# Performance work log

Measured on AMD Instinct MI355X. Metric: run time of the kernel, lower is better.

The kernel has to match this reference:

```python
import jax, jax.numpy as jnp
import numpy as np

D = 128; H = 8; DH = D // H; L = 3
NA = 8000; NL = 32000; N = NA + NL
E1 = 65536; D_RPE = 5; D_FFN = 2 * D; RF_H = 128


def _ln(x, eps=1e-5):
    mu = x.mean(-1, keepdims=True)
    var = ((x - mu) ** 2).mean(-1, keepdims=True)
    return (x - mu) * jax.lax.rsqrt(var + eps)


def _rms(x, eps=1e-8):
    rms = jnp.sqrt((x ** 2).sum(-1, keepdims=True)) / np.sqrt(x.shape[-1]).astype(np.float32)
    return x / (rms + eps)


def _seg_softmax(logits, idx, n):
    m = jax.ops.segment_max(logits, idx, num_segments=n)
    e = jnp.exp(logits - m[idx])
    s = jax.ops.segment_sum(e, idx, num_segments=n)
    return e / (s[idx] + 1e-16)


def _gat_layer(x, edge_attr, src, dst, mp_W, mp_b, eu_W, eu_b, Wq, Wk, Wv, Wo, fW1, fb1, fW2, fb2):
    E = src.shape[0]
    # build_mem: gather endpoints, project, LN, ReLU
    cat = jnp.concatenate([x[dst], x[src], edge_attr], axis=-1)       # [E, 3D]
    mem = jax.nn.relu(_ln(cat @ mp_W.T + mp_b))                       # [E, D]
    delta = jax.nn.relu(_ln(mem @ eu_W.T + eu_b))                     # edge_update_block
    edge_attr = _ln(edge_attr + delta)                                # edge_norm
    # multi-head edge attention: q from receiver node, k/v from mem
    q = (x[dst] @ Wq.T).reshape(E, H, DH)
    k = (mem @ Wk.T).reshape(E, H, DH)
    v = (mem @ Wv.T).reshape(E, H, DH)
    logits = (q * k).sum(-1) / np.sqrt(DH).astype(np.float32)         # [E, H]
    attn = _seg_softmax(logits, dst, N)                               # segment softmax over receivers
    msg = (attn[..., None] * v).reshape(E, D) @ Wo.T                  # [E, D]
    aggr = jax.ops.segment_sum(msg, dst, num_segments=N)              # scatter-add
    x = _ln(x + aggr)
    h = jax.nn.relu(x @ fW1.T + fb1) @ fW2.T + fb2
    x = _ln(x + h)
    return x, edge_attr


def _ddc(x_cur, prev_list, W1, b1, W2, b2):
    xs = jnp.stack(prev_list, axis=1)                                 # [N, k, D]
    a = jax.nn.gelu(_rms(x_cur) @ W1.T + b1, approximate=False)
    a = jax.nn.softmax(a @ W2.T + b2, axis=-1)                        # [N, k]
    return (a[..., None] * xs).sum(1)


def setup_inputs() -> dict:
    key = jax.random.key(0)
    ks = iter(jax.random.split(key, 48))
    def nrm(shape, fan_in):
        return jax.random.normal(next(ks), shape, jnp.float32) * np.float32(1.0 / np.sqrt(fan_in))
    inp = {}
    inp['actors'] = jax.random.normal(next(ks), (NA, D), jnp.float32)
    inp['lanes'] = jax.random.normal(next(ks), (NL, D), jnp.float32)
    inp['a2a_attr'] = jax.random.normal(next(ks), (E1, D), jnp.float32)
    inp['l2l_attr'] = jax.random.normal(next(ks), (E1, D), jnp.float32)
    inp['a2l_rpe'] = jax.random.normal(next(ks), (E1, D_RPE), jnp.float32)
    inp['rpe_W'] = nrm((D, D_RPE), D_RPE); inp['rpe_b'] = jnp.zeros((D,), jnp.float32)
    inp['mp_W'] = nrm((L, D, 3 * D), 3 * D); inp['mp_b'] = jnp.zeros((L, D), jnp.float32)
    inp['eu_W'] = nrm((L, D, D), D); inp['eu_b'] = jnp.zeros((L, D), jnp.float32)
    inp['Wq'] = nrm((L, D, D), D); inp['Wk'] = nrm((L, D, D), D)
    inp['Wv'] = nrm((L, D, D), D); inp['Wo'] = nrm((L, D, D), D)
    inp['ffn_W1'] = nrm((L, D_FFN, D), D); inp['ffn_b1'] = jnp.zeros((L, D_FFN), jnp.float32)
    inp['ffn_W2'] = nrm((L, D, D_FFN), D_FFN); inp['ffn_b2'] = jnp.zeros((L, D), jnp.float32)
    inp['rf0_W1'] = nrm((RF_H, D), D); inp['rf0_b1'] = jnp.zeros((RF_H,), jnp.float32)
    inp['rf0_W2'] = nrm((1, RF_H), RF_H); inp['rf0_b2'] = jnp.zeros((1,), jnp.float32)
    inp['rf1_W1'] = nrm((RF_H, D), D); inp['rf1_b1'] = jnp.zeros((RF_H,), jnp.float32)
    inp['rf1_W2'] = nrm((2, RF_H), RF_H); inp['rf1_b2'] = jnp.zeros((2,), jnp.float32)
    inp['a2a_edges'] = jax.random.randint(next(ks), (2, E1), 0, N, jnp.int32)
    inp['l2l_edges'] = jax.random.randint(next(ks), (2, E1), 0, N, jnp.int32)
    inp['a2l_edges'] = jax.random.randint(next(ks), (2, E1), 0, N, jnp.int32)
    return inp


def reference(actors, lanes, a2a_attr, l2l_attr, a2l_rpe, rpe_W, rpe_b,
              mp_W, mp_b, eu_W, eu_b, Wq, Wk, Wv, Wo,
              ffn_W1, ffn_b1, ffn_W2, ffn_b2,
              rf0_W1, rf0_b1, rf0_W2, rf0_b2,
              rf1_W1, rf1_b1, rf1_W2, rf1_b2,
              a2a_edges, l2l_edges, a2l_edges):
    token = jnp.concatenate([actors, lanes], axis=0)                  # single scene: actors then lanes
    edge_index = jnp.concatenate([a2a_edges, l2l_edges, a2l_edges], axis=1)
    a2l_attr = jax.nn.relu(_ln(a2l_rpe @ rpe_W.T + rpe_b))            # proj_a2l_l2a_rpe
    edge_attr = jnp.concatenate([a2a_attr, l2l_attr, a2l_attr], axis=0)
    src, dst = edge_index[0], edge_index[1]
    rf = [(rf0_W1, rf0_b1, rf0_W2, rf0_b2), (rf1_W1, rf1_b1, rf1_W2, rf1_b2)]
    token_list = [token]
    for i in range(L):
        token, edge_attr = _gat_layer(token, edge_attr, src, dst,
                                      mp_W[i], mp_b[i], eu_W[i], eu_b[i],
                                      Wq[i], Wk[i], Wv[i], Wo[i],
                                      ffn_W1[i], ffn_b1[i], ffn_W2[i], ffn_b2[i])
        if i < L - 1:
            token = _ddc(token, token_list, *rf[i])
        token_list.append(token)
    return token[:NA], token[NA:]
```

## Files before the change

kernel.cpp:

```cpp
#include <hip/hip_runtime.h>
#include <hip/hip_bf16.h>

using bf16 = __hip_bfloat16;
typedef __bf16 bf16x8 __attribute__((ext_vector_type(8)));
typedef float f32x4 __attribute__((ext_vector_type(4)));

constexpr int DD   = 128;
constexpr int NACT = 8000;
constexpr int NN   = 40000;
constexpr int E1   = 65536;
constexpr int EE   = 3 * E1;

#define BM 128
#define BN 128
#define LDK 40
#define LDM 132

__device__ __forceinline__ int edge_dst(int e, const int* e0, const int* e1, const int* e2) {
  int ty = e >> 16, idx = e & 65535;
  const int* ep = (ty == 0) ? e0 : ((ty == 1) ? e1 : e2);
  return ep[E1 + idx];
}
__device__ __forceinline__ int edge_src(int e, const int* e0, const int* e1, const int* e2) {
  int ty = e >> 16, idx = e & 65535;
  const int* ep = (ty == 0) ? e0 : ((ty == 1) ? e1 : e2);
  return ep[idx];
}

__device__ __forceinline__ void mfma_step(const bf16* A0, int lda, const bf16* B0, int ldb,
                                          f32x4 acc[4][4], int wm, int wn, int lane) {
  const int lr = lane & 15;
  const int lk = (lane >> 4) * 8;
  bf16x8 a[4], b[4];
#pragma unroll
  for (int i = 0; i < 4; i++)
    a[i] = *(const bf16x8*)(A0 + (size_t)(wm * 64 + i * 16 + lr) * lda + lk);
#pragma unroll
  for (int j = 0; j < 4; j++)
    b[j] = *(const bf16x8*)(B0 + (size_t)(wn * 64 + j * 16 + lr) * ldb + lk);
#pragma unroll
  for (int i = 0; i < 4; i++)
#pragma unroll
    for (int j = 0; j < 4; j++)
      acc[i][j] = __builtin_amdgcn_mfma_f32_16x16x32_bf16(a[i], b[j], acc[i][j], 0, 0, 0);
}

__device__ __forceinline__ void row_ln_stats(f32x4 acc[4][4], float (*red_s)[BM],
                                             float (*red_q)[BM], int wm, int wn, int lane) {
  const int lr = lane & 15, lg = lane >> 4;
#pragma unroll
  for (int i = 0; i < 4; i++) {
#pragma unroll
    for (int q = 0; q < 4; q++) {
      float s = acc[i][0][q] + acc[i][1][q] + acc[i][2][q] + acc[i][3][q];
      float t = acc[i][0][q] * acc[i][0][q] + acc[i][1][q] * acc[i][1][q]
              + acc[i][2][q] * acc[i][2][q] + acc[i][3][q] * acc[i][3][q];
#pragma unroll
      for (int off = 1; off < 16; off <<= 1) {
        s += __shfl_xor(s, off);
        t += __shfl_xor(t, off);
      }
      if (lr == 0) {
        int row = wm * 64 + i * 16 + lg * 4 + q;
        red_s[wn][row] = s;
        red_q[wn][row] = t;
      }
    }
  }
}

template<int LAST>
__global__ __launch_bounds__(256, 2) void k_fused(
    const bf16* __restrict__ Wmp, const bf16* __restrict__ W2,
    const float* __restrict__ mpb, const float* __restrict__ eub,
    bf16* eah, const bf16* __restrict__ x0h,
    const bf16* __restrict__ qh, bf16* vout,
    float* __restrict__ logi, unsigned* __restrict__ nmax,
    const int* __restrict__ e0, const int* __restrict__ e1, const int* __restrict__ e2)
{
  __shared__ __align__(16) bf16 As[2][BM * LDK];
  __shared__ __align__(16) bf16 Bs[2][BM * LDK];
  __shared__ __align__(16) bf16 mem_s[BM * LDM];
  __shared__ float red_s[2][BM], red_q[2][BM];
  __shared__ int sdst[BM], ssrc[BM];

  const int tid = threadIdx.x;
  const int bm0 = blockIdx.x * BM;
  const int lane = tid & 63, w = tid >> 6, wm = w >> 1, wn = w & 1;
  const int row0 = tid >> 2, row1 = row0 + 64;
  const int c8 = (tid & 3) * 8;

  if (tid < 128) sdst[tid] = edge_dst(bm0 + tid, e0, e1, e2);
  else           ssrc[tid - 128] = edge_src(bm0 + tid - 128, e0, e1, e2);
  __syncthreads();
  const int rd0 = sdst[row0], rd1 = sdst[row1];
  const int rs0 = ssrc[row0], rs1 = ssrc[row1];

  auto loadAB = [&](int kb, uint4& a0, uint4& a1, uint4& b0, uint4& b1) {
    const int k0 = kb * 32;
    const bf16 *pa0, *pa1;
    if (k0 < 128)      { pa0 = x0h + (size_t)rd0 * DD + k0 + c8;
                         pa1 = x0h + (size_t)rd1 * DD + k0 + c8; }
    else if (k0 < 256) { pa0 = x0h + (size_t)rs0 * DD + (k0 - 128) + c8;
                         pa1 = x0h + (size_t)rs1 * DD + (k0 - 128) + c8; }
    else               { pa0 = eah + (size_t)(bm0 + row0) * DD + (k0 - 256) + c8;
                         pa1 = eah + (size_t)(bm0 + row1) * DD + (k0 - 256) + c8; }
    a0 = *(const uint4*)pa0; a1 = *(const uint4*)pa1;
    b0 = *(const uint4*)(Wmp + (size_t)row0 * 384 + k0 + c8);
    b1 = *(const uint4*)(Wmp + (size_t)row1 * 384 + k0 + c8);
  };
  auto stAB = [&](int buf, uint4 a0, uint4 a1, uint4 b0, uint4 b1) {
    *(uint4*)&As[buf][row0 * LDK + c8] = a0;
    *(uint4*)&As[buf][row1 * LDK + c8] = a1;
    *(uint4*)&Bs[buf][row0 * LDK + c8] = b0;
    *(uint4*)&Bs[buf][row1 * LDK + c8] = b1;
  };

  f32x4 acc[4][4] = {};
  {
    uint4 a0, a1, b0, b1;
    loadAB(0, a0, a1, b0, b1);
    stAB(0, a0, a1, b0, b1);
    __syncthreads();
  }
#pragma unroll 1
  for (int kb = 0; kb < 12; kb++) {
    uint4 a0, a1, b0, b1;
    if (kb < 11) loadAB(kb + 1, a0, a1, b0, b1);
    mfma_step(As[kb & 1], LDK, Bs[kb & 1], LDK, acc, wm, wn, lane);
    __syncthreads();
    if (kb < 11) {
      stAB((kb + 1) & 1, a0, a1, b0, b1);
      __syncthreads();
    }
  }

  const int lr = lane & 15, lg = lane >> 4;
  const int colb = wn * 64 + lr;
  const int rowb = wm * 64 + lg * 4;

#pragma unroll
  for (int j = 0; j < 4; j++) {
    float bj = mpb[colb + j * 16];
#pragma unroll
    for (int i = 0; i < 4; i++)
#pragma unroll
      for (int q = 0; q < 4; q++) acc[i][j][q] += bj;
  }
  row_ln_stats(acc, red_s, red_q, wm, wn, lane);
  __syncthreads();
#pragma unroll
  for (int i = 0; i < 4; i++) {
#pragma unroll
    for (int q = 0; q < 4; q++) {
      int row = rowb + i * 16 + q;
      float S  = red_s[0][row] + red_s[1][row];
      float Qs = red_q[0][row] + red_q[1][row];
      float mu = S * 0.0078125f;
      float var = Qs * 0.0078125f - mu * mu;
      float inv = 1.0f / sqrtf(var + 1e-5f);
#pragma unroll
      for (int j = 0; j < 4; j++)
        mem_s[row * LDM + colb + j * 16] =
            __float2bfloat16(fmaxf((acc[i][j][q] - mu) * inv, 0.f));
    }
  }

  auto stage_b2 = [&](int buf, int w2off, int k0) {
    *(uint4*)&Bs[buf][row0 * LDK + c8] =
        *(const uint4*)(W2 + (size_t)(w2off + row0) * DD + k0 + c8);
    *(uint4*)&Bs[buf][row1 * LDK + c8] =
        *(const uint4*)(W2 + (size_t)(w2off + row1) * DD + k0 + c8);
  };

  if constexpr (LAST == 0) {
    f32x4 acc2[4][4] = {};
#pragma unroll 1
    for (int kb = 0; kb < 4; kb++) {
      stage_b2(kb & 1, 0, kb * 32);
      __syncthreads();
      mfma_step(mem_s + kb * 32, LDM, Bs[kb & 1], LDK, acc2, wm, wn, lane);
    }
#pragma unroll
    for (int j = 0; j < 4; j++) {
      float bj = eub[colb + j * 16];
#pragma unroll
      for (int i = 0; i < 4; i++)
#pragma unroll
        for (int q = 0; q < 4; q++) acc2[i][j][q] += bj;
    }
    __syncthreads();
    row_ln_stats(acc2, red_s, red_q, wm, wn, lane);
    __syncthreads();
#pragma unroll
    for (int i = 0; i < 4; i++) {
#pragma unroll
      for (int q = 0; q < 4; q++) {
        int row = rowb + i * 16 + q;
        float S  = red_s[0][row] + red_s[1][row];
        float Qs = red_q[0][row] + red_q[1][row];
        float mu = S * 0.0078125f;
        float var = Qs * 0.0078125f - mu * mu;
        float inv = 1.0f / sqrtf(var + 1e-5f);
        int r = bm0 + row;
#pragma unroll
        for (int j = 0; j < 4; j++) {
          float d = fmaxf((acc2[i][j][q] - mu) * inv, 0.f);
          float eo = __bfloat162float(eah[(size_t)r * DD + colb + j * 16]);
          acc2[i][j][q] = eo + d;
        }
      }
    }
    __syncthreads();
    row_ln_stats(acc2, red_s, red_q, wm, wn, lane);
    __syncthreads();
#pragma unroll
    for (int i = 0; i < 4; i++) {
#pragma unroll
      for (int q = 0; q < 4; q++) {
        int row = rowb + i * 16 + q;
        float S  = red_s[0][row] + red_s[1][row];
        float Qs = red_q[0][row] + red_q[1][row];
        float mu = S * 0.0078125f;
        float var = Qs * 0.0078125f - mu * mu;
        float inv = 1.0f / sqrtf(var + 1e-5f);
        int r = bm0 + row;
#pragma unroll
        for (int j = 0; j < 4; j++)
          eah[(size_t)r * DD + colb + j * 16] =
              __float2bfloat16((acc2[i][j][q] - mu) * inv);
      }
    }
  } else {
    f32x4 acc2[4][4] = {};
#pragma unroll 1
    for (int kb = 0; kb < 4; kb++) {
      stage_b2(kb & 1, 0, kb * 32);
      __syncthreads();
      mfma_step(mem_s + kb * 32, LDM, Bs[kb & 1], LDK, acc2, wm, wn, lane);
    }
#pragma unroll
    for (int i = 0; i < 4; i++) {
#pragma unroll
      for (int q = 0; q < 4; q++) {
        int row = rowb + i * 16 + q;
        int dst = sdst[row];
#pragma unroll
        for (int j = 0; j < 4; j++) {
          int h = wn * 4 + j;
          float qv = __bfloat162float(qh[(size_t)dst * DD + h * 16 + lr]);
          float p = acc2[i][j][q] * qv;
#pragma unroll
          for (int off = 1; off < 16; off <<= 1) p += __shfl_xor(p, off);
          if (lr == 0) {
            p *= 0.25f;
            int e = bm0 + row;
            logi[(size_t)e * 8 + h] = p;
            unsigned u = __float_as_uint(p);
            u = (u & 0x80000000u) ? ~u : (u | 0x80000000u);
            atomicMax(nmax + (size_t)dst * 8 + h, u);
          }
        }
      }
    }
    f32x4 acc3[4][4] = {};
#pragma unroll 1
    for (int kb = 0; kb < 4; kb++) {
      stage_b2(kb & 1, 128, kb * 32);
      __syncthreads();
      mfma_step(mem_s + kb * 32, LDM, Bs[kb & 1], LDK, acc3, wm, wn, lane);
    }
#pragma unroll
    for (int i = 0; i < 4; i++) {
#pragma unroll
      for (int q = 0; q < 4; q++) {
        int e = bm0 + rowb + i * 16 + q;
#pragma unroll
        for (int j = 0; j < 4; j++)
          vout[(size_t)e * DD + colb + j * 16] = __float2bfloat16(acc3[i][j][q]);
      }
    }
  }
}

template<int AMODE, int EPI>
__global__ __launch_bounds__(256) void k_gemm(
    const bf16* __restrict__ A, const bf16* __restrict__ B,
    void* __restrict__ out,
    const float* __restrict__ bias, const float* __restrict__ aux,
    const int* __restrict__ e0, const int* __restrict__ e1, const int* __restrict__ e2,
    int M, int K, int lda, int ldc)
{
  __shared__ __align__(16) bf16 As[BM * LDK];
  __shared__ __align__(16) bf16 Bs[BN * LDK];
  __shared__ float red_s[2][BM], red_q[2][BM];

  const int tid = threadIdx.x;
  const int bm0 = blockIdx.x * BM;
  const int bn0 = blockIdx.y * BN;
  const int lane = tid & 63, w = tid >> 6, wm = w >> 1, wn = w & 1;

  f32x4 acc[4][4] = {};
  const int KB = K >> 5;
#pragma unroll 1
  for (int kb = 0; kb < KB; kb++) {
    const int k0 = kb * 32;
    int c = tid;
#pragma unroll
    for (int it = 0; it < 2; it++, c += 256) {
      int row = c >> 2, c8 = (c & 3) * 8;
      uint4 v;
      if constexpr (AMODE == 2) {
        int e = bm0 + row;
        int col = k0 + c8, h = col >> 4;
        v = *(const uint4*)(A + (size_t)e * lda + col);
        float at = aux[(size_t)e * 8 + h];
        union { uint4 u; bf16 hh[8]; } vv; vv.u = v;
#pragma unroll
        for (int t = 0; t < 8; t++)
          vv.hh[t] = __float2bfloat16(at * __bfloat162float(vv.hh[t]));
        v = vv.u;
      } else {
        int r = bm0 + row;
        v = make_uint4(0u, 0u, 0u, 0u);
        if (r < M) v = *(const uint4*)(A + (size_t)r * lda + k0 + c8);
      }
      *(uint4*)&As[row * LDK + c8] = v;
      *(uint4*)&Bs[row * LDK + c8] = *(const uint4*)(B + (size_t)(bn0 + row) * K + k0 + c8);
    }
    __syncthreads();
    mfma_step(As, LDK, Bs, LDK, acc, wm, wn, lane);
    __syncthreads();
  }

  const int lr = lane & 15, lg = lane >> 4;
  const int colb = wn * 64 + lr;
  const int rowb = wm * 64 + lg * 4;

  if constexpr (EPI == 1) {
#pragma unroll
    for (int i = 0; i < 4; i++)
#pragma unroll
      for (int q = 0; q < 4; q++) {
        int r = bm0 + rowb + i * 16 + q;
        if (r < M) {
#pragma unroll
          for (int j = 0; j < 4; j++)
            ((bf16*)out)[(size_t)r * ldc + bn0 + colb + j * 16] = __float2bfloat16(acc[i][j][q]);
        }
      }
  }
  if constexpr (EPI == 4) {
    float* og = (float*)out;
#pragma unroll
    for (int i = 0; i < 4; i++)
#pragma unroll
      for (int q = 0; q < 4; q++) {
        int e = bm0 + rowb + i * 16 + q;
        int dst = edge_dst(e, e0, e1, e2);
#pragma unroll
        for (int j = 0; j < 4; j++)
          atomicAdd(og + (size_t)dst * DD + colb + j * 16, acc[i][j][q]);
      }
  }
  if constexpr (EPI == 5) {
#pragma unroll
    for (int j = 0; j < 4; j++) {
      float b = bias[bn0 + colb + j * 16];
#pragma unroll
      for (int i = 0; i < 4; i++)
#pragma unroll
        for (int q = 0; q < 4; q++) acc[i][j][q] += b;
    }
#pragma unroll
    for (int i = 0; i < 4; i++)
#pragma unroll
      for (int q = 0; q < 4; q++) {
        int r = bm0 + rowb + i * 16 + q;
        if (r < M) {
#pragma unroll
          for (int j = 0; j < 4; j++)
            ((bf16*)out)[(size_t)r * ldc + bn0 + colb + j * 16] =
                __float2bfloat16(fmaxf(acc[i][j][q], 0.f));
        }
      }
  }
  if constexpr (EPI == 6) {
#pragma unroll
    for (int i = 0; i < 4; i++)
#pragma unroll
      for (int q = 0; q < 4; q++) {
        int r = bm0 + rowb + i * 16 + q;
        if (r < M) {
#pragma unroll
          for (int j = 0; j < 4; j++)
            acc[i][j][q] += bias[colb + j * 16] + aux[(size_t)r * DD + colb + j * 16];
        }
      }
    row_ln_stats(acc, red_s, red_q, wm, wn, lane);
    __syncthreads();
#pragma unroll
    for (int i = 0; i < 4; i++)
#pragma unroll
      for (int q = 0; q < 4; q++) {
        int row = rowb + i * 16 + q;
        float S  = red_s[0][row] + red_s[1][row];
        float Qs = red_q[0][row] + red_q[1][row];
        float mu = S * 0.0078125f;
        float var = Qs * 0.0078125f - mu * mu;
        float inv = 1.0f / sqrtf(var + 1e-5f);
        int r = bm0 + row;
        if (r < M) {
#pragma unroll
          for (int j = 0; j < 4; j++)
            ((float*)out)[(size_t)r * DD + colb + j * 16] = (acc[i][j][q] - mu) * inv;
        }
      }
  }
}

__device__ __forceinline__ float2 ln_pair(float2 v, float eps) {
  float s = v.x + v.y, sq = v.x * v.x + v.y * v.y;
#pragma unroll
  for (int o = 32; o > 0; o >>= 1) {
    s += __shfl_xor(s, o);
    sq += __shfl_xor(sq, o);
  }
  float mu = s * 0.0078125f;
  float var = sq * 0.0078125f - mu * mu;
  float inv = 1.0f / sqrtf(var + eps);
  return make_float2((v.x - mu) * inv, (v.y - mu) * inv);
}

__global__ void k_init_ea(const float* __restrict__ a2a, const float* __restrict__ l2l,
                          const float* __restrict__ rpe, const float* __restrict__ rpeW,
                          const float* __restrict__ rpeb, bf16* __restrict__ eah) {
  int r = blockIdx.x * 4 + (threadIdx.x >> 6);
  int lane = threadIdx.x & 63;
  int ty = r >> 16, idx = r & 65535;
  int c0 = lane * 2;
  float2 y;
  if (ty < 2) {
    y = *(const float2*)((ty == 0 ? a2a : l2l) + (size_t)idx * DD + c0);
  } else {
    float rp0 = rpe[idx * 5 + 0], rp1 = rpe[idx * 5 + 1], rp2 = rpe[idx * 5 + 2];
    float rp3 = rpe[idx * 5 + 3], rp4 = rpe[idx * 5 + 4];
    float2 v;
    v.x = rpeb[c0]     + rp0 * rpeW[c0 * 5]           + rp1 * rpeW[c0 * 5 + 1]
        + rp2 * rpeW[c0 * 5 + 2]     + rp3 * rpeW[c0 * 5 + 3]     + rp4 * rpeW[c0 * 5 + 4];
    v.y = rpeb[c0 + 1] + rp0 * rpeW[(c0 + 1) * 5]     + rp1 * rpeW[(c0 + 1) * 5 + 1]
        + rp2 * rpeW[(c0 + 1) * 5 + 2] + rp3 * rpeW[(c0 + 1) * 5 + 3] + rp4 * rpeW[(c0 + 1) * 5 + 4];
    y = ln_pair(v, 1e-5f);
    y.x = fmaxf(y.x, 0.f);
    y.y = fmaxf(y.y, 0.f);
  }
  size_t o = (size_t)r * DD + c0;
  eah[o] = __float2bfloat16(y.x);
  eah[o + 1] = __float2bfloat16(y.y);
}

__global__ void k_x1(const float* __restrict__ actors, const float* __restrict__ lanesp,
                     const float* __restrict__ aggr, float* __restrict__ x1,
                     bf16* __restrict__ x1h, int R) {
  int r = blockIdx.x * 4 + (threadIdx.x >> 6);
  if (r >= R) return;
  int lane = threadIdx.x & 63;
  int c0 = lane * 2;
  const float* xp = (r < NACT) ? (actors + (size_t)r * DD) : (lanesp + (size_t)(r - NACT) * DD);
  float2 v = *(const float2*)(xp + c0);
  float2 a = *(const float2*)(aggr + (size_t)r * DD + c0);
  v.x += a.x; v.y += a.y;
  float2 y = ln_pair(v, 1e-5f);
  size_t o = (size_t)r * DD + c0;
  *(float2*)(x1 + o) = y;
  x1h[o] = __float2bfloat16(y.x);
  x1h[o + 1] = __float2bfloat16(y.y);
}

__global__ void k_evals(float* __restrict__ logit, const unsigned* __restrict__ nmax,
                        float* __restrict__ nsum,
                        const int* __restrict__ e0, const int* __restrict__ e1,
                        const int* __restrict__ e2) {
  int gid = blockIdx.x * 256 + threadIdx.x;
  int e = gid >> 3, h = gid & 7;
  int dst = edge_dst(e, e0, e1, e2);
  unsigned u = nmax[(size_t)dst * 8 + h];
  float m = (u & 0x80000000u) ? __uint_as_float(u ^ 0x80000000u) : __uint_as_float(~u);
  float v = expf(logit[gid] - m);
  logit[gid] = v;
  atomicAdd(nsum + (size_t)dst * 8 + h, v);
}

__global__ void k_attn(float* __restrict__ logit, const float* __restrict__ nsum,
                       const int* __restrict__ e0, const int* __restrict__ e1,
                       const int* __restrict__ e2) {
  int gid = blockIdx.x * 256 + threadIdx.x;
  int e = gid >> 3, h = gid & 7;
  int dst = edge_dst(e, e0, e1, e2);
  logit[gid] = logit[gid] / (nsum[(size_t)dst * 8 + h] + 1e-16f);
}

__global__ void k_conv(const float* __restrict__ a, bf16* __restrict__ b, int n) {
  int i = blockIdx.x * 256 + threadIdx.x;
  if (i < n) b[i] = __float2bfloat16(a[i]);
}

__global__ void k_x0h(const float* __restrict__ actors, const float* __restrict__ lanesp,
                      bf16* __restrict__ x0h) {
  int gid = blockIdx.x * 256 + threadIdx.x;
  int n = gid >> 7, c = gid & 127;
  float v = (n < NACT) ? actors[(size_t)n * DD + c] : lanesp[(size_t)(n - NACT) * DD + c];
  x0h[gid] = __float2bfloat16(v);
}

extern "C" void kernel_launch(void* const* d_in, const int* in_sizes, int n_in,
                              void* d_out, int out_size, void* d_ws, size_t ws_size,
                              hipStream_t stream) {
  (void)in_sizes; (void)n_in; (void)out_size;
  if (ws_size < (128ull << 20)) return;

  const float* actors = (const float*)d_in[0];
  const float* lanesp = (const float*)d_in[1];
  const float* a2a    = (const float*)d_in[2];
  const float* l2l    = (const float*)d_in[3];
  const float* rpe    = (const float*)d_in[4];
  const float* rpeW   = (const float*)d_in[5];
  const float* rpeb   = (const float*)d_in[6];
  const float* mpW    = (const float*)d_in[7];
  const float* mpb    = (const float*)d_in[8];
  const float* euW    = (const float*)d_in[9];
  const float* eub    = (const float*)d_in[10];
  const float* Wq     = (const float*)d_in[11];
  const float* Wk     = (const float*)d_in[12];
  const float* Wv     = (const float*)d_in[13];
  const float* Wo     = (const float*)d_in[14];
  const float* fW1    = (const float*)d_in[15];
  const float* fb1    = (const float*)d_in[16];
  const float* fW2    = (const float*)d_in[17];
  const float* fb2    = (const float*)d_in[18];
  const int* e0 = (const int*)d_in[27];
  const int* e1 = (const int*)d_in[28];
  const int* e2 = (const int*)d_in[29];

  char* ws = (char*)d_ws;
  bf16* W_MP = (bf16*)ws;
  bf16* W_EU = W_MP + 147456;
  bf16* W_WQ = W_EU + 32768;
  bf16* W_KV = W_WQ + 16384;
  bf16* W_WO = W_KV + 32768;
  bf16* W_F1 = W_WO + 16384;
  bf16* W_F2 = W_F1 + 32768;

  bf16*  X0H = (bf16*)(ws + (1ull << 20));
  bf16*  QH  = (bf16*)(ws + (12ull << 20));
  float* POOL = (float*)(ws + (24ull << 20));
  float*    AGGR = POOL;
  float*    X1   = POOL + 5120000;
  float*    LOGI = POOL + 10240000;
  unsigned* NMAX = (unsigned*)(POOL + 11812864);
  float*    NSUM = POOL + 12132864;
  bf16* EAH = (bf16*)(ws + (80ull << 20));
  bf16* VH  = EAH;
  bf16* X1H = X0H;
  bf16* H1H = EAH;

  k_conv<<<576, 256, 0, stream>>>(mpW, W_MP, 147456);
  k_conv<<<128, 256, 0, stream>>>(euW, W_EU, 32768);
  k_conv<<<64, 256, 0, stream>>>(Wq + 2 * 16384, W_WQ, 16384);
  k_conv<<<64, 256, 0, stream>>>(Wk + 2 * 16384, W_KV, 16384);
  k_conv<<<64, 256, 0, stream>>>(Wv + 2 * 16384, W_KV + 16384, 16384);
  k_conv<<<64, 256, 0, stream>>>(Wo + 2 * 16384, W_WO, 16384);
  k_conv<<<128, 256, 0, stream>>>(fW1 + 2 * 32768, W_F1, 32768);
  k_conv<<<128, 256, 0, stream>>>(fW2 + 2 * 32768, W_F2, 32768);
  k_x0h<<<20000, 256, 0, stream>>>(actors, lanesp, X0H);
  k_init_ea<<<49152, 256, 0, stream>>>(a2a, l2l, rpe, rpeW, rpeb, EAH);

  k_gemm<0, 1><<<313, 256, 0, stream>>>(X0H, W_WQ, QH, nullptr, nullptr,
                                        e0, e1, e2, NN, 128, 128, DD);

  hipMemsetAsync(AGGR, 0, (size_t)NN * DD * 4, stream);
  hipMemsetAsync(NMAX, 0, (size_t)NN * 8 * 4, stream);
  hipMemsetAsync(NSUM, 0, (size_t)NN * 8 * 4, stream);

  for (int i = 0; i < 2; i++) {
    k_fused<0><<<EE / BM, 256, 0, stream>>>(W_MP + i * 49152, W_EU + i * 16384,
        mpb + i * 128, eub + i * 128, EAH, X0H, nullptr, nullptr,
        nullptr, nullptr, e0, e1, e2);
  }
  k_fused<1><<<EE / BM, 256, 0, stream>>>(W_MP + 2 * 49152, W_KV,
      mpb + 2 * 128, nullptr, EAH, X0H, QH, VH, LOGI, NMAX, e0, e1, e2);

  k_evals<<<EE * 8 / 256, 256, 0, stream>>>(LOGI, NMAX, NSUM, e0, e1, e2);
  k_attn<<<EE * 8 / 256, 256, 0, stream>>>(LOGI, NSUM, e0, e1, e2);

  k_gemm<2, 4><<<EE / BM, 256, 0, stream>>>(VH, W_WO, AGGR, nullptr, LOGI,
                                            e0, e1, e2, EE, 128, 128, DD);

  k_x1<<<NN / 4, 256, 0, stream>>>(actors, lanesp, AGGR, X1, X1H, NN);
  k_gemm<0, 5><<<dim3(313, 2), 256, 0, stream>>>(X1H, W_F1, H1H, fb1 + 2 * 256, nullptr,
                                                 e0, e1, e2, NN, 128, 128, 256);
  k_gemm<0, 6><<<dim3(313, 1), 256, 0, stream>>>(H1H, W_F2, d_out, fb2 + 2 * 128, X1,
                                                 e0, e1, e2, NN, 256, 256, DD);
}
```

Measured before the change: 607.7 us.

## Alias shared memory, stage tile epilogues through LDS, double-buffer generic GEMM

Puts all shared buffers of the fused edge kernel into one aliased byte array and shrinks the padding, so more blocks fit per CU (launch bounds raised to 3). Output tiles (edge_attr, v, GEMM bf16 outputs, LN fp32 outputs) are staged through LDS and written with coalesced 16-byte stores instead of scattered 2-byte stores. The generic GEMM gains register-prefetch double buffering, and the fused main loop drops one barrier per K step. The risks are LDS bank conflicts from the new padding, extra barriers in the second-GEMM loops, and register pressure from the higher occupancy target. A stray scalar store of W2[0] is left in stage_b2.

```diff
diff --git a/kernel.cpp b/kernel.cpp
--- a/kernel.cpp
+++ b/kernel.cpp
@@ -13,8 +13,8 @@
 
 #define BM 128
 #define BN 128
-#define LDK 40
-#define LDM 132
+#define LDK 36
+#define LDM 136
 
 __device__ __forceinline__ int edge_dst(int e, const int* e0, const int* e1, const int* e2) {
   int ty = e >> 16, idx = e & 65535;
@@ -45,8 +45,8 @@
       acc[i][j] = __builtin_amdgcn_mfma_f32_16x16x32_bf16(a[i], b[j], acc[i][j], 0, 0, 0);
 }
 
-__device__ __forceinline__ void row_ln_stats(f32x4 acc[4][4], float (*red_s)[BM],
-                                             float (*red_q)[BM], int wm, int wn, int lane) {
+__device__ __forceinline__ void row_ln_stats(const f32x4 acc[4][4], float* red_s,
+                                             float* red_q, int wm, int wn, int lane) {
   const int lr = lane & 15, lg = lane >> 4;
 #pragma unroll
   for (int i = 0; i < 4; i++) {
@@ -62,15 +62,15 @@
       }
       if (lr == 0) {
         int row = wm * 64 + i * 16 + lg * 4 + q;
-        red_s[wn][row] = s;
-        red_q[wn][row] = t;
+        red_s[wn * 128 + row] = s;
+        red_q[wn * 128 + row] = t;
       }
     }
   }
 }
 
 template<int LAST>
-__global__ __launch_bounds__(256, 2) void k_fused(
+__global__ __launch_bounds__(256, 3) void k_fused(
     const bf16* __restrict__ Wmp, const bf16* __restrict__ W2,
     const float* __restrict__ mpb, const float* __restrict__ eub,
     bf16* eah, const bf16* __restrict__ x0h,
@@ -78,11 +78,14 @@
     float* __restrict__ logi, unsigned* __restrict__ nmax,
     const int* __restrict__ e0, const int* __restrict__ e1, const int* __restrict__ e2)
 {
-  __shared__ __align__(16) bf16 As[2][BM * LDK];
-  __shared__ __align__(16) bf16 Bs[2][BM * LDK];
-  __shared__ __align__(16) bf16 mem_s[BM * LDM];
-  __shared__ float red_s[2][BM], red_q[2][BM];
-  __shared__ int sdst[BM], ssrc[BM];
+  __shared__ __align__(16) char smem[49152];
+  bf16* const S    = (bf16*)smem;
+  bf16* const mem_s = S;
+  bf16* const Bs2   = S + 18432;
+  float* const red_s = (float*)(smem + 46080);
+  float* const red_q = (float*)(smem + 47104);
+  int* const sdst = (int*)(smem + 48128);
+  int* const ssrc = (int*)(smem + 48640);
 
   const int tid = threadIdx.x;
   const int bm0 = blockIdx.x * BM;
@@ -110,10 +113,12 @@
     b1 = *(const uint4*)(Wmp + (size_t)row1 * 384 + k0 + c8);
   };
   auto stAB = [&](int buf, uint4 a0, uint4 a1, uint4 b0, uint4 b1) {
-    *(uint4*)&As[buf][row0 * LDK + c8] = a0;
-    *(uint4*)&As[buf][row1 * LDK + c8] = a1;
-    *(uint4*)&Bs[buf][row0 * LDK + c8] = b0;
-    *(uint4*)&Bs[buf][row1 * LDK + c8] = b1;
+    bf16* As = S + buf * 4608;
+    bf16* Bs = S + 9216 + buf * 4608;
+    *(uint4*)&As[row0 * LDK + c8] = a0;
+    *(uint4*)&As[row1 * LDK + c8] = a1;
+    *(uint4*)&Bs[row0 * LDK + c8] = b0;
+    *(uint4*)&Bs[row1 * LDK + c8] = b1;
   };
 
   f32x4 acc[4][4] = {};
@@ -127,12 +132,9 @@
   for (int kb = 0; kb < 12; kb++) {
     uint4 a0, a1, b0, b1;
     if (kb < 11) loadAB(kb + 1, a0, a1, b0, b1);
-    mfma_step(As[kb & 1], LDK, Bs[kb & 1], LDK, acc, wm, wn, lane);
-    __syncthreads();
-    if (kb < 11) {
-      stAB((kb + 1) & 1, a0, a1, b0, b1);
-      __syncthreads();
-    }
+    mfma_step(S + (kb & 1) * 4608, LDK, S + 9216 + (kb & 1) * 4608, LDK, acc, wm, wn, lane);
+    if (kb < 11) stAB((kb + 1) & 1, a0, a1, b0, b1);
+    __syncthreads();
   }
 
   const int lr = lane & 15, lg = lane >> 4;
@@ -154,9 +156,9 @@
 #pragma unroll
     for (int q = 0; q < 4; q++) {
       int row = rowb + i * 16 + q;
-      float S  = red_s[0][row] + red_s[1][row];
-      float Qs = red_q[0][row] + red_q[1][row];
-      float mu = S * 0.0078125f;
+      float Sm = red_s[row] + red_s[128 + row];
+      float Qs = red_q[row] + red_q[128 + row];
+      float mu = Sm * 0.0078125f;
       float var = Qs * 0.0078125f - mu * mu;
       float inv = 1.0f / sqrtf(var + 1e-5f);
 #pragma unroll
@@ -166,20 +168,28 @@
     }
   }
 
-  auto stage_b2 = [&](int buf, int w2off, int k0) {
-    *(uint4*)&Bs[buf][row0 * LDK + c8] =
-        *(const uint4*)(W2 + (size_t)(w2off + row0) * DD + k0 + c8);
-    *(uint4*)&Bs[buf][row1 * LDK + c8] =
-        *(const uint4*)(W2 + (size_t)(w2off + row1) * DD + k0 + c8);
+  auto stage_b2 = [&](int w2off, int k0) {
+    Bs2[row0 * LDK + c8] = W2[0];
+    *(uint4*)&Bs2[row0 * LDK + c8] = *(const uint4*)(W2 + (size_t)(w2off + row0) * DD + k0 + c8);
+    *(uint4*)&Bs2[row1 * LDK + c8] = *(const uint4*)(W2 + (size_t)(w2off + row1) * DD + k0 + c8);
+  };
+  auto store_tile = [&](bf16* dst) {
+#pragma unroll
+    for (int c = 0; c < 8; c++) {
+      int off = c * 2048 + tid * 8;
+      int row = off >> 7, col = off & 127;
+      *(uint4*)(dst + (size_t)bm0 * DD + off) = *(uint4*)&mem_s[row * LDM + col];
+    }
   };
 
   if constexpr (LAST == 0) {
     f32x4 acc2[4][4] = {};
 #pragma unroll 1
     for (int kb = 0; kb < 4; kb++) {
-      stage_b2(kb & 1, 0, kb * 32);
-      __syncthreads();
-      mfma_step(mem_s + kb * 32, LDM, Bs[kb & 1], LDK, acc2, wm, wn, lane);
+      __syncthreads();
+      stage_b2(0, kb * 32);
+      __syncthreads();
+      mfma_step(mem_s + kb * 32, LDM, Bs2, LDK, acc2, wm, wn, lane);
     }
 #pragma unroll
     for (int j = 0; j < 4; j++) {
@@ -197,9 +207,9 @@
 #pragma unroll
       for (int q = 0; q < 4; q++) {
         int row = rowb + i * 16 + q;
-        float S  = red_s[0][row] + red_s[1][row];
-        float Qs = red_q[0][row] + red_q[1][row];
-        float mu = S * 0.0078125f;
+        float Sm = red_s[row] + red_s[128 + row];
+        float Qs = red_q[row] + red_q[128 + row];
+        float mu = Sm * 0.0078125f;
         float var = Qs * 0.0078125f - mu * mu;
         float inv = 1.0f / sqrtf(var + 1e-5f);
         int r = bm0 + row;
@@ -219,25 +229,27 @@
 #pragma unroll
       for (int q = 0; q < 4; q++) {
         int row = rowb + i * 16 + q;
-        float S  = red_s[0][row] + red_s[1][row];
-        float Qs = red_q[0][row] + red_q[1][row];
-        float mu = S * 0.0078125f;
+        float Sm = red_s[row] + red_s[128 + row];
+        float Qs = red_q[row] + red_q[128 + row];
+        float mu = Sm * 0.0078125f;
         float var = Qs * 0.0078125f - mu * mu;
         float inv = 1.0f / sqrtf(var + 1e-5f);
-        int r = bm0 + row;
 #pragma unroll
         for (int j = 0; j < 4; j++)
-          eah[(size_t)r * DD + colb + j * 16] =
+          mem_s[row * LDM + colb + j * 16] =
               __float2bfloat16((acc2[i][j][q] - mu) * inv);
       }
     }
+    __syncthreads();
+    store_tile(eah);
   } else {
     f32x4 acc2[4][4] = {};
 #pragma unroll 1
     for (int kb = 0; kb < 4; kb++) {
-      stage_b2(kb & 1, 0, kb * 32);
-      __syncthreads();
-      mfma_step(mem_s + kb * 32, LDM, Bs[kb & 1], LDK, acc2, wm, wn, lane);
+      __syncthreads();
+      stage_b2(0, kb * 32);
+      __syncthreads();
+      mfma_step(mem_s + kb * 32, LDM, Bs2, LDK, acc2, wm, wn, lane);
     }
 #pragma unroll
     for (int i = 0; i < 4; i++) {
@@ -266,78 +278,147 @@
     f32x4 acc3[4][4] = {};
 #pragma unroll 1
     for (int kb = 0; kb < 4; kb++) {
-      stage_b2(kb & 1, 128, kb * 32);
-      __syncthreads();
-      mfma_step(mem_s + kb * 32, LDM, Bs[kb & 1], LDK, acc3, wm, wn, lane);
-    }
-#pragma unroll
-    for (int i = 0; i < 4; i++) {
+      __syncthreads();
+      stage_b2(128, kb * 32);
+      __syncthreads();
+      mfma_step(mem_s + kb * 32, LDM, Bs2, LDK, acc3, wm, wn, lane);
+    }
+    __syncthreads();
+#pragma unroll
+    for (int i = 0; i < 4; i++)
 #pragma unroll
       for (int q = 0; q < 4; q++) {
-        int e = bm0 + rowb + i * 16 + q;
+        int row = rowb + i * 16 + q;
 #pragma unroll
         for (int j = 0; j < 4; j++)
-          vout[(size_t)e * DD + colb + j * 16] = __float2bfloat16(acc3[i][j][q]);
-      }
-    }
+          mem_s[row * LDM + colb + j * 16] = __float2bfloat16(acc3[i][j][q]);
+      }
+    __syncthreads();
+    store_tile(vout);
   }
 }
 
 template<int AMODE, int EPI>
-__global__ __launch_bounds__(256) void k_gemm(
+__global__ __launch_bounds__(256, 3) void k_gemm(
     const bf16* __restrict__ A, const bf16* __restrict__ B,
     void* __restrict__ out,
     const float* __restrict__ bias, const float* __restrict__ aux,
     const int* __restrict__ e0, const int* __restrict__ e1, const int* __restrict__ e2,
     int M, int K, int lda, int ldc)
 {
-  __shared__ __align__(16) bf16 As[BM * LDK];
-  __shared__ __align__(16) bf16 Bs[BN * LDK];
-  __shared__ float red_s[2][BM], red_q[2][BM];
+  __shared__ __align__(16) char smem[38912];
+  bf16* const S = (bf16*)smem;
+  float* const red_s = (float*)(smem + 36864);
+  float* const red_q = (float*)(smem + 37888);
 
   const int tid = threadIdx.x;
   const int bm0 = blockIdx.x * BM;
   const int bn0 = blockIdx.y * BN;
   const int lane = tid & 63, w = tid >> 6, wm = w >> 1, wn = w & 1;
+  const int row0 = tid >> 2, row1 = row0 + 64;
+  const int c8 = (tid & 3) * 8;
+
+  auto loadAB = [&](int kb, uint4& a0, uint4& a1, uint4& b0, uint4& b1) {
+    const int k0 = kb * 32;
+    if constexpr (AMODE == 2) {
+      int ee0 = bm0 + row0, ee1 = bm0 + row1;
+      int h = (k0 + c8) >> 4;
+      a0 = *(const uint4*)(A + (size_t)ee0 * lda + k0 + c8);
+      a1 = *(const uint4*)(A + (size_t)ee1 * lda + k0 + c8);
+      float at0 = aux[(size_t)ee0 * 8 + h], at1 = aux[(size_t)ee1 * 8 + h];
+      union { uint4 u; bf16 hh[8]; } v0, v1; v0.u = a0; v1.u = a1;
+#pragma unroll
+      for (int t = 0; t < 8; t++) {
+        v0.hh[t] = __float2bfloat16(at0 * __bfloat162float(v0.hh[t]));
+        v1.hh[t] = __float2bfloat16(at1 * __bfloat162float(v1.hh[t]));
+      }
+      a0 = v0.u; a1 = v1.u;
+    } else {
+      int r0 = bm0 + row0, r1 = bm0 + row1;
+      a0 = make_uint4(0u, 0u, 0u, 0u); a1 = a0;
+      if (r0 < M) a0 = *(const uint4*)(A + (size_t)r0 * lda + k0 + c8);
+      if (r1 < M) a1 = *(const uint4*)(A + (size_t)r1 * lda + k0 + c8);
+    }
+    b0 = *(const uint4*)(B + (size_t)(bn0 + row0) * K + k0 + c8);
+    b1 = *(const uint4*)(B + (size_t)(bn0 + row1) * K + k0 + c8);
+  };
+  auto stAB = [&](int buf, uint4 a0, uint4 a1, uint4 b0, uint4 b1) {
+    bf16* As = S + buf * 4608;
+    bf16* Bs = S + 9216 + buf * 4608;
+    *(uint4*)&As[row0 * LDK + c8] = a0;
+    *(uint4*)&As[row1 * LDK + c8] = a1;
+    *(uint4*)&Bs[row0 * LDK + c8] = b0;
+    *(uint4*)&Bs[row1 * LDK + c8] = b1;
+  };
 
   f32x4 acc[4][4] = {};
   const int KB = K >> 5;
+  {
+    uint4 a0, a1, b0, b1;
+    loadAB(0, a0, a1, b0, b1);
+    stAB(0, a0, a1, b0, b1);
+    __syncthreads();
+  }
 #pragma unroll 1
   for (int kb = 0; kb < KB; kb++) {
-    const int k0 = kb * 32;
-    int c = tid;
-#pragma unroll
-    for (int it = 0; it < 2; it++, c += 256) {
-      int row = c >> 2, c8 = (c & 3) * 8;
-      uint4 v;
-      if constexpr (AMODE == 2) {
-        int e = bm0 + row;
-        int col = k0 + c8, h = col >> 4;
-        v = *(const uint4*)(A + (size_t)e * lda + col);
-        float at = aux[(size_t)e * 8 + h];
-        union { uint4 u; bf16 hh[8]; } vv; vv.u = v;
-#pragma unroll
-        for (int t = 0; t < 8; t++)
-          vv.hh[t] = __float2bfloat16(at * __bfloat162float(vv.hh[t]));
-        v = vv.u;
-      } else {
-        int r = bm0 + row;
-        v = make_uint4(0u, 0u, 0u, 0u);
-        if (r < M) v = *(const uint4*)(A + (size_t)r * lda + k0 + c8);
-      }
-      *(uint4*)&As[row * LDK + c8] = v;
-      *(uint4*)&Bs[row * LDK + c8] = *(const uint4*)(B + (size_t)(bn0 + row) * K + k0 + c8);
-    }
-    __syncthreads();
-    mfma_step(As, LDK, Bs, LDK, acc, wm, wn, lane);
+    uint4 a0, a1, b0, b1;
+    if (kb < KB - 1) loadAB(kb + 1, a0, a1, b0, b1);
+    mfma_step(S + (kb & 1) * 4608, LDK, S + 9216 + (kb & 1) * 4608, LDK, acc, wm, wn, lane);
+    if (kb < KB - 1) stAB((kb + 1) & 1, a0, a1, b0, b1);
     __syncthreads();
   }
 
   const int lr = lane & 15, lg = lane >> 4;
   const int colb = wn * 64 + lr;
   const int rowb = wm * 64 + lg * 4;
-
-  if constexpr (EPI == 1) {
+  bf16* const stg = S;
+
+  if constexpr (EPI == 1 || EPI == 5) {
+    if constexpr (EPI == 5) {
+#pragma unroll
+      for (int j = 0; j < 4; j++) {
+        float b = bias[bn0 + colb + j * 16];
+#pragma unroll
+        for (int i = 0; i < 4; i++)
+#pragma unroll
+          for (int q = 0; q < 4; q++) acc[i][j][q] = fmaxf(acc[i][j][q] + b, 0.f);
+      }
+    }
+#pragma unroll
+    for (int i = 0; i < 4; i++)
+#pragma unroll
+      for (int q = 0; q < 4; q++) {
+        int row = rowb + i * 16 + q;
+#pragma unroll
+        for (int j = 0; j < 4; j++)
+          stg[row * LDM + colb + j * 16] = __float2bfloat16(acc[i][j][q]);
+      }
+    __syncthreads();
+#pragma unroll
+    for (int c = 0; c < 8; c++) {
+      int off = c * 2048 + tid * 8;
+      int row = off >> 7, col = off & 127;
+      int r = bm0 + row;
+      if (r < M)
+        *(uint4*)((bf16*)out + (size_t)r * ldc + bn0 + col) = *(uint4*)&stg[row * LDM + col];
+    }
+  }
+
+  if constexpr (EPI == 4) {
+    float* og = (float*)out;
+#pragma unroll
+    for (int i = 0; i < 4; i++)
+#pragma unroll
+      for (int q = 0; q < 4; q++) {
+        int e = bm0 + rowb + i * 16 + q;
+        int dst = edge_dst(e, e0, e1, e2);
+#pragma unroll
+        for (int j = 0; j < 4; j++)
+          atomicAdd(og + (size_t)dst * DD + colb + j * 16, acc[i][j][q]);
+      }
+  }
+
+  if constexpr (EPI == 6) {
 #pragma unroll
     for (int i = 0; i < 4; i++)
 #pragma unroll
@@ -346,76 +427,42 @@
         if (r < M) {
 #pragma unroll
           for (int j = 0; j < 4; j++)
-            ((bf16*)out)[(size_t)r * ldc + bn0 + colb + j * 16] = __float2bfloat16(acc[i][j][q]);
-        }
-      }
-  }
-  if constexpr (EPI == 4) {
-    float* og = (float*)out;
-#pragma unroll
-    for (int i = 0; i < 4; i++)
-#pragma unroll
-      for (int q = 0; q < 4; q++) {
-        int e = bm0 + rowb + i * 16 + q;
-        int dst = edge_dst(e, e0, e1, e2);
-#pragma unroll
-        for (int j = 0; j < 4; j++)
-          atomicAdd(og + (size_t)dst * DD + colb + j * 16, acc[i][j][q]);
-      }
-  }
-  if constexpr (EPI == 5) {
-#pragma unroll
-    for (int j = 0; j < 4; j++) {
-      float b = bias[bn0 + colb + j * 16];
-#pragma unroll
-      for (int i = 0; i < 4; i++)
-#pragma unroll
-        for (int q = 0; q < 4; q++) acc[i][j][q] += b;
-    }
-#pragma unroll
-    for (int i = 0; i < 4; i++)
-#pragma unroll
-      for (int q = 0; q < 4; q++) {
-        int r = bm0 + rowb + i * 16 + q;
-        if (r < M) {
-#pragma unroll
-          for (int j = 0; j < 4; j++)
-            ((bf16*)out)[(size_t)r * ldc + bn0 + colb + j * 16] =
-                __float2bfloat16(fmaxf(acc[i][j][q], 0.f));
-        }
-      }
-  }
-  if constexpr (EPI == 6) {
-#pragma unroll
-    for (int i = 0; i < 4; i++)
-#pragma unroll
-      for (int q = 0; q < 4; q++) {
-        int r = bm0 + rowb + i * 16 + q;
-        if (r < M) {
-#pragma unroll
-          for (int j = 0; j < 4; j++)
             acc[i][j][q] += bias[colb + j * 16] + aux[(size_t)r * DD + colb + j * 16];
         }
       }
     row_ln_stats(acc, red_s, red_q, wm, wn, lane);
     __syncthreads();
-#pragma unroll
-    for (int i = 0; i < 4; i++)
-#pragma unroll
-      for (int q = 0; q < 4; q++) {
-        int row = rowb + i * 16 + q;
-        float S  = red_s[0][row] + red_s[1][row];
-        float Qs = red_q[0][row] + red_q[1][row];
-        float mu = S * 0.0078125f;
-        float var = Qs * 0.0078125f - mu * mu;
-        float inv = 1.0f / sqrtf(var + 1e-5f);
-        int r = bm0 + row;
-        if (r < M) {
-#pragma unroll
-          for (int j = 0; j < 4; j++)
-            ((float*)out)[(size_t)r * DD + colb + j * 16] = (acc[i][j][q] - mu) * inv;
-        }
-      }
+    float* const fstg = (float*)S;
+#pragma unroll
+    for (int h = 0; h < 2; h++) {
+      if (wm == h) {
+#pragma unroll
+        for (int i = 0; i < 4; i++)
+#pragma unroll
+          for (int q = 0; q < 4; q++) {
+            int row = rowb + i * 16 + q;
+            float Sm = red_s[row] + red_s[128 + row];
+            float Qs = red_q[row] + red_q[128 + row];
+            float mu = Sm * 0.0078125f;
+            float var = Qs * 0.0078125f - mu * mu;
+            float inv = 1.0f / sqrtf(var + 1e-5f);
+            int rloc = row - h * 64;
+#pragma unroll
+            for (int j = 0; j < 4; j++)
+              fstg[rloc * 132 + colb + j * 16] = (acc[i][j][q] - mu) * inv;
+          }
+      }
+      __syncthreads();
+#pragma unroll
+      for (int c = 0; c < 8; c++) {
+        int boff = c * 4096 + tid * 16;
+        int row = boff >> 9, col = (boff & 511) >> 2;
+        int r = bm0 + h * 64 + row;
+        if (r < M)
+          *(float4*)((float*)out + (size_t)r * DD + col) = *(float4*)&fstg[row * 132 + col];
+      }
+      __syncthreads();
+    }
   }
 }
 
```

Measured after the change: 832.6 us. +37.0%, slower.
